# Optimization experiments

Measured on AMD Instinct MI355X. Metric: run time of the kernel, lower is better.

The kernel has to match this reference:

```python
import jax, jax.numpy as jnp
import numpy as np

B, N, D = 8, 2048, 512
DK, DV = 512, 512


def setup_inputs() -> dict:
    key = jax.random.key(0)
    ks = jax.random.split(key, 7)
    s = 1.0 / np.sqrt(D)
    return {
        "x": jax.random.normal(ks[0], (B, N, D), dtype=jnp.float32),
        "Wq": jax.random.normal(ks[1], (D, DK), dtype=jnp.float32) * s,
        "bq": jnp.zeros((DK,), dtype=jnp.float32),
        "Wk": jax.random.normal(ks[2], (D, DK), dtype=jnp.float32) * s,
        "bk": jnp.zeros((DK,), dtype=jnp.float32),
        "Wv": jax.random.normal(ks[3], (D, DV), dtype=jnp.float32) * s,
        "bv": jnp.zeros((DV,), dtype=jnp.float32),
    }


def reference(x, Wq, bq, Wk, bk, Wv, bv):
    # norm = 1/sqrt(dim_k); original divides softmax output by norm (post-softmax scale)
    inv_norm = jnp.sqrt(jnp.asarray(DK, dtype=x.dtype))  # 1/norm = sqrt(dim_k)
    Q = x @ Wq + bq  # [B,N,DK]
    K = x @ Wk + bk  # [B,N,DK]
    V = x @ Wv + bv  # [B,N,DV]
    scores = jnp.einsum("bnd,bmd->bnm", Q, K)  # [B,N,N] (NO pre-softmax scaling)
    att = jax.nn.softmax(scores, axis=-1) * inv_norm  # faithful post-softmax scale
    return jnp.einsum("bnm,bmv->bnv", att, V)  # [B,N,DV]
```

## Files before the change

kernel.cpp:

```cpp
#include <hip/hip_runtime.h>
#include <stdint.h>
#include <stddef.h>


typedef _Float16 f16_t;
typedef _Float16 f16x8 __attribute__((ext_vector_type(8)));
typedef float    f32x4 __attribute__((ext_vector_type(4)));

__device__ __forceinline__ f32x4 mfma_h(f16x8 a, f16x8 b, f32x4 c) {
  return __builtin_amdgcn_mfma_f32_16x16x32_f16(a, b, c, 0, 0, 0);
}

__device__ __forceinline__ void gl_lds16(const void* g, void* lds) {
  __builtin_amdgcn_global_load_lds(
      (const __attribute__((address_space(1))) unsigned int*)g,
      (__attribute__((address_space(3))) unsigned int*)lds, 16, 0, 0);
}

__device__ __forceinline__ void stage_tile(f16_t* lds, const f16_t* g,
                                           size_t gstride, int wave, int lane) {
  const int l8 = lane >> 3;
  const int lslot = (lane & 7) ^ l8;
  #pragma unroll
  for (int c = 0; c < 4; ++c) {
    const int chunk = wave * 4 + c;
    const int row = chunk * 8 + l8;
    gl_lds16(g + (size_t)row * gstride + lslot * 8, lds + chunk * 512);
  }
}

__device__ __forceinline__ f16x8 lds_frag(const f16_t* buf, int R, int slot) {
  return *(const f16x8*)&buf[R * 64 + (((slot ^ (R & 7)) & 7) << 3)];
}

__device__ __forceinline__ unsigned int fenc(float f) {
  unsigned int u = __float_as_uint(f);
  return (u & 0x80000000u) ? ~u : (u | 0x80000000u);
}
__device__ __forceinline__ float fdec(unsigned int e) {
  unsigned int u = (e & 0x80000000u) ? (e & 0x7fffffffu) : ~e;
  return __uint_as_float(u);
}

__device__ __forceinline__ int xcd_swz(int id, int nwg) {
  return (id & 7) * (nwg >> 3) + (id >> 3);
}

__global__ __launch_bounds__(256) void k_conv_x(const float* __restrict__ x,
                                                f16_t* __restrict__ x16) {
  const int i = (blockIdx.x * 256 + threadIdx.x) * 8;
  const float4 a = *(const float4*)&x[i];
  const float4 b = *(const float4*)&x[i + 4];
  float v[8] = {a.x, a.y, a.z, a.w, b.x, b.y, b.z, b.w};
  f16x8 h;
  #pragma unroll
  for (int j = 0; j < 8; ++j) h[j] = (f16_t)v[j];
  *(f16x8*)&x16[i] = h;
}

__global__ __launch_bounds__(256) void k_conv_w(const float* __restrict__ Wq,
                                                const float* __restrict__ Wk,
                                                const float* __restrict__ Wv,
                                                f16_t* __restrict__ Wt) {
  __shared__ float t[64][65];
  const int p = blockIdx.z;
  const float* __restrict__ W = (p == 0) ? Wq : (p == 1) ? Wk : Wv;
  const int n0 = blockIdx.x * 64, k0 = blockIdx.y * 64;
  const int tx = threadIdx.x & 63, ty = threadIdx.x >> 6;
  #pragma unroll
  for (int j = 0; j < 16; ++j)
    t[ty * 16 + j][tx] = W[(size_t)(k0 + ty * 16 + j) * 512 + n0 + tx];
  __syncthreads();
  #pragma unroll
  for (int j = 0; j < 16; ++j) {
    const int nl = ty * 16 + j;
    Wt[(size_t)p * 262144 + (size_t)(n0 + nl) * 512 + k0 + tx] =
        (f16_t)t[tx][nl];
  }
}

__global__ __launch_bounds__(256, 2) void k_proj(
    const f16_t* __restrict__ x16, const f16_t* __restrict__ Wt,
    const float* __restrict__ bq, const float* __restrict__ bk,
    const float* __restrict__ bv,
    f16_t* __restrict__ Q, f16_t* __restrict__ K, f16_t* __restrict__ Vt)
{
  __shared__ __align__(16) unsigned char smem[34816];
  f16_t* A = (f16_t*)smem;
  f16_t* B = (f16_t*)(smem + 16384);

  const int wg = xcd_swz(blockIdx.x, 1536);
  const int mt = wg / 12, jt = wg % 12;
  const int which = jt >> 2;
  const int jb = (jt & 3) * 128;

  const int tid = threadIdx.x, lane = tid & 63, wave = tid >> 6;
  const int wr = wave >> 1, wc = wave & 1, l15 = lane & 15, lg = lane >> 4;
  const int rowbase = mt * 128;

  const f16_t* Wbase = Wt + (size_t)which * 262144 + (size_t)jb * 512;

  f32x4 acc[4][4] = {};

  for (int kb = 0; kb < 512; kb += 64) {
    __syncthreads();
    stage_tile(A, x16 + (size_t)rowbase * 512 + kb, 512, wave, lane);
    stage_tile(B, Wbase + kb, 512, wave, lane);
    __syncthreads();
    #pragma unroll
    for (int h = 0; h < 2; ++h) {
      const int slot0 = h * 4 + lg;
      f16x8 af[4], bf[4];
      #pragma unroll
      for (int g = 0; g < 4; ++g) {
        af[g] = lds_frag(A, wr * 64 + g * 16 + l15, slot0);
        bf[g] = lds_frag(B, wc * 64 + g * 16 + l15, slot0);
      }
      #pragma unroll
      for (int i = 0; i < 4; ++i)
        #pragma unroll
        for (int j = 0; j < 4; ++j)
          acc[i][j] = mfma_h(af[i], bf[j], acc[i][j]);
    }
  }

  if (which != 2) {
    f16_t* __restrict__ O = (which == 0) ? Q : K;
    const float* __restrict__ bb = (which == 0) ? bq : bk;
    #pragma unroll
    for (int j = 0; j < 4; ++j) {
      const int jl = jb + wc * 64 + j * 16 + l15;
      const float bias = bb[jl];
      #pragma unroll
      for (int i = 0; i < 4; ++i)
        #pragma unroll
        for (int r = 0; r < 4; ++r) {
          const int row = rowbase + wr * 64 + i * 16 + lg * 4 + r;
          O[(size_t)row * 512 + jl] = (f16_t)(acc[i][j][r] + bias);
        }
    }
  } else {
    __syncthreads();
    f16_t* vtl = (f16_t*)smem;
    #pragma unroll
    for (int j = 0; j < 4; ++j) {
      const int jj = wc * 64 + j * 16 + l15;
      const float bias = bv[jb + jj];
      #pragma unroll
      for (int i = 0; i < 4; ++i)
        #pragma unroll
        for (int r = 0; r < 4; ++r) {
          const int ii = wr * 64 + i * 16 + lg * 4 + r;
          vtl[jj * 136 + ii] = (f16_t)(acc[i][j][r] + bias);
        }
    }
    __syncthreads();
    const int dv = tid >> 1, hf = tid & 1;
    const int bat = rowbase >> 11, n0 = rowbase & 2047;
    f16_t* __restrict__ dst =
        &Vt[((size_t)bat * 512 + jb + dv) * 2048 + n0 + hf * 64];
    const f16_t* src = &vtl[dv * 136 + hf * 64];
    #pragma unroll
    for (int s = 0; s < 8; ++s)
      *(f16x8*)&dst[s * 8] = *(const f16x8*)&src[s * 8];
  }
}

__global__ __launch_bounds__(256, 2) void k_qk(const f16_t* __restrict__ Q,
                                               const f16_t* __restrict__ K,
                                               float* __restrict__ S,
                                               unsigned int* __restrict__ mEnc)
{
  __shared__ __align__(16) f16_t A[128 * 64];
  __shared__ __align__(16) f16_t Bt[128 * 64];

  const int wg = xcd_swz(blockIdx.x, 2048);
  const int bat = wg >> 8, mt = (wg >> 4) & 15, nt = wg & 15;
  const int tid = threadIdx.x, lane = tid & 63, wave = tid >> 6;
  const int wr = wave >> 1, wc = wave & 1, l15 = lane & 15, lg = lane >> 4;

  f32x4 acc[4][4] = {};
  const f16_t* Abase = Q + ((size_t)bat * 2048 + mt * 128) * 512;
  const f16_t* Bbase = K + ((size_t)bat * 2048 + nt * 128) * 512;

  for (int kb = 0; kb < 512; kb += 64) {
    __syncthreads();
    stage_tile(A, Abase + kb, 512, wave, lane);
    stage_tile(Bt, Bbase + kb, 512, wave, lane);
    __syncthreads();
    #pragma unroll
    for (int h = 0; h < 2; ++h) {
      const int slot0 = h * 4 + lg;
      f16x8 af[4], bf[4];
      #pragma unroll
      for (int g = 0; g < 4; ++g) {
        af[g] = lds_frag(A, wr * 64 + g * 16 + l15, slot0);
        bf[g] = lds_frag(Bt, wc * 64 + g * 16 + l15, slot0);
      }
      #pragma unroll
      for (int i = 0; i < 4; ++i)
        #pragma unroll
        for (int j = 0; j < 4; ++j)
          acc[i][j] = mfma_h(af[i], bf[j], acc[i][j]);
    }
  }

  #pragma unroll
  for (int i = 0; i < 4; ++i)
    #pragma unroll
    for (int r = 0; r < 4; ++r) {
      const int ii = mt * 128 + wr * 64 + i * 16 + lg * 4 + r;
      float mv = fmaxf(fmaxf(acc[i][0][r], acc[i][1][r]),
                       fmaxf(acc[i][2][r], acc[i][3][r]));
      mv = fmaxf(mv, __shfl_xor(mv, 1));
      mv = fmaxf(mv, __shfl_xor(mv, 2));
      mv = fmaxf(mv, __shfl_xor(mv, 4));
      mv = fmaxf(mv, __shfl_xor(mv, 8));
      if (l15 == 0)
        atomicMax(&mEnc[(size_t)bat * 2048 + ii], fenc(mv));
      #pragma unroll
      for (int j = 0; j < 4; ++j) {
        const int jj = nt * 128 + wc * 64 + j * 16 + l15;
        S[((size_t)bat * 2048 + ii) * 2048 + jj] = acc[i][j][r];
      }
    }
}

__global__ __launch_bounds__(256, 2) void k_pv2(const float* __restrict__ S,
                                                const f16_t* __restrict__ Vt,
                                                const unsigned int* __restrict__ mEnc,
                                                float* __restrict__ out)
{
  __shared__ __align__(16) f16_t P[64 * 64];
  __shared__ __align__(16) f16_t Vl[256 * 64];
  __shared__ float lred[64][4];

  const int id = blockIdx.x;
  const int bat = id & 7, qt = (id >> 3) & 31, dvh = id >> 8;
  const int tid = threadIdx.x, lane = tid & 63, wave = tid >> 6;
  const int l15 = lane & 15, lg = lane >> 4;

  const int qs = tid >> 2;
  const int cq = tid & 3;
  const float mrow = fdec(mEnc[bat * 2048 + qt * 64 + qs]);
  const float* __restrict__ srow =
      S + ((size_t)bat * 2048 + qt * 64 + qs) * 2048;
  const f16_t* Vbase = Vt + ((size_t)bat * 512 + dvh * 256) * 2048;

  f32x4 acc[4][4] = {};
  float l_part = 0.f;

  for (int kb = 0; kb < 2048; kb += 64) {
    __syncthreads();
    stage_tile(Vl, Vbase + kb, 2048, wave, lane);
    stage_tile(Vl + 128 * 64, Vbase + (size_t)128 * 2048 + kb, 2048, wave, lane);
    #pragma unroll
    for (int s2 = 0; s2 < 2; ++s2) {
      const int kv0 = cq * 16 + s2 * 8;
      const float4 a = *(const float4*)&srow[kb + kv0];
      const float4 b = *(const float4*)&srow[kb + kv0 + 4];
      float e[8] = {a.x, a.y, a.z, a.w, b.x, b.y, b.z, b.w};
      f16x8 p;
      #pragma unroll
      for (int j = 0; j < 8; ++j) {
        const float ev = __expf(e[j] - mrow);
        l_part += ev;
        p[j] = (f16_t)ev;
      }
      const int slot = cq * 2 + s2;
      *(f16x8*)&P[qs * 64 + ((slot ^ (qs & 7)) << 3)] = p;
    }
    __syncthreads();
    #pragma unroll
    for (int ks = 0; ks < 2; ++ks) {
      const int slot0 = ks * 4 + lg;
      f16x8 af[4], bf[4];
      #pragma unroll
      for (int g = 0; g < 4; ++g) {
        af[g] = lds_frag(P, g * 16 + l15, slot0);
        bf[g] = lds_frag(Vl, wave * 64 + g * 16 + l15, slot0);
      }
      #pragma unroll
      for (int i = 0; i < 4; ++i)
        #pragma unroll
        for (int j = 0; j < 4; ++j)
          acc[i][j] = mfma_h(af[i], bf[j], acc[i][j]);
    }
  }

  __syncthreads();
  lred[qs][cq] = l_part;
  __syncthreads();

  #pragma unroll
  for (int i = 0; i < 4; ++i)
    #pragma unroll
    for (int r = 0; r < 4; ++r) {
      const int ql = i * 16 + lg * 4 + r;
      const float l = lred[ql][0] + lred[ql][1] + lred[ql][2] + lred[ql][3];
      const float sc = 22.62741699796952f / l;
      const size_t orow = ((size_t)bat * 2048 + qt * 64 + ql) * 512;
      #pragma unroll
      for (int j = 0; j < 4; ++j) {
        const int dv = dvh * 256 + wave * 64 + j * 16 + l15;
        out[orow + dv] = acc[i][j][r] * sc;
      }
    }
}

extern "C" void kernel_launch(void* const* d_in, const int* in_sizes, int n_in,
                              void* d_out, int out_size, void* d_ws, size_t ws_size,
                              hipStream_t stream) {
  const float* x  = (const float*)d_in[0];
  const float* Wq = (const float*)d_in[1];
  const float* bq = (const float*)d_in[2];
  const float* Wk = (const float*)d_in[3];
  const float* bk = (const float*)d_in[4];
  const float* Wv = (const float*)d_in[5];
  const float* bv = (const float*)d_in[6];
  float* out = (float*)d_out;

  char* ws = (char*)d_ws;
  f16_t* x16 = (f16_t*)(ws + 0);
  f16_t* Q   = (f16_t*)(ws + 16777216);
  f16_t* K   = (f16_t*)(ws + 33554432);
  f16_t* Vt  = (f16_t*)(ws + 50331648);
  float* S   = (float*)(ws + 67108864);
  f16_t* Wt  = (f16_t*)(ws + 201326592);
  unsigned int* mEnc = (unsigned int*)(ws + 202899456);

  hipMemsetAsync(mEnc, 0, 65536, stream);
  k_conv_x<<<4096, 256, 0, stream>>>(x, x16);
  k_conv_w<<<dim3(8, 8, 3), 256, 0, stream>>>(Wq, Wk, Wv, Wt);
  k_proj<<<1536, 256, 0, stream>>>(x16, Wt, bq, bk, bv, Q, K, Vt);
  k_qk<<<2048, 256, 0, stream>>>(Q, K, S, mEnc);
  k_pv2<<<512, 256, 0, stream>>>(S, Vt, mEnc, out);
}
```

Before: 160.1 us.

## Compute tile-local softmax in QK kernel and store fp16 probabilities with per-tile stats

New measurement: 159.0 us. About the same (-0.7%).

```diff
diff --git a/kernel.cpp b/kernel.cpp
--- a/kernel.cpp
+++ b/kernel.cpp
@@ -29,17 +29,20 @@
   }
 }
 
+__device__ __forceinline__ void stage_tile64(f16_t* lds, const f16_t* g,
+                                             size_t gstride, int wave, int lane) {
+  const int l8 = lane >> 3;
+  const int lslot = (lane & 7) ^ l8;
+  #pragma unroll
+  for (int c = 0; c < 2; ++c) {
+    const int chunk = wave * 2 + c;
+    const int row = chunk * 8 + l8;
+    gl_lds16(g + (size_t)row * gstride + lslot * 8, lds + chunk * 512);
+  }
+}
+
 __device__ __forceinline__ f16x8 lds_frag(const f16_t* buf, int R, int slot) {
   return *(const f16x8*)&buf[R * 64 + (((slot ^ (R & 7)) & 7) << 3)];
-}
-
-__device__ __forceinline__ unsigned int fenc(float f) {
-  unsigned int u = __float_as_uint(f);
-  return (u & 0x80000000u) ? ~u : (u | 0x80000000u);
-}
-__device__ __forceinline__ float fdec(unsigned int e) {
-  unsigned int u = (e & 0x80000000u) ? (e & 0x7fffffffu) : ~e;
-  return __uint_as_float(u);
 }
 
 __device__ __forceinline__ int xcd_swz(int id, int nwg) {
@@ -166,13 +169,17 @@
   }
 }
 
-__global__ __launch_bounds__(256, 2) void k_qk(const f16_t* __restrict__ Q,
-                                               const f16_t* __restrict__ K,
-                                               float* __restrict__ S,
-                                               unsigned int* __restrict__ mEnc)
+__global__ __launch_bounds__(256, 2) void k_qk2(const f16_t* __restrict__ Q,
+                                                const f16_t* __restrict__ K,
+                                                f16_t* __restrict__ P,
+                                                float* __restrict__ mG,
+                                                float* __restrict__ lG)
 {
-  __shared__ __align__(16) f16_t A[128 * 64];
-  __shared__ __align__(16) f16_t Bt[128 * 64];
+  __shared__ __align__(16) unsigned char smem[34816];
+  f16_t* A  = (f16_t*)smem;
+  f16_t* Bt = (f16_t*)(smem + 16384);
+  __shared__ float redm[128][2];
+  __shared__ float redl[128][2];
 
   const int wg = xcd_swz(blockIdx.x, 2048);
   const int bat = wg >> 8, mt = (wg >> 4) & 15, nt = wg & 15;
@@ -205,100 +212,159 @@
     }
   }
 
+  const float LOG2E = 1.4426950408889634f;
   #pragma unroll
   for (int i = 0; i < 4; ++i)
     #pragma unroll
     for (int r = 0; r < 4; ++r) {
-      const int ii = mt * 128 + wr * 64 + i * 16 + lg * 4 + r;
       float mv = fmaxf(fmaxf(acc[i][0][r], acc[i][1][r]),
                        fmaxf(acc[i][2][r], acc[i][3][r]));
       mv = fmaxf(mv, __shfl_xor(mv, 1));
       mv = fmaxf(mv, __shfl_xor(mv, 2));
       mv = fmaxf(mv, __shfl_xor(mv, 4));
       mv = fmaxf(mv, __shfl_xor(mv, 8));
-      if (l15 == 0)
-        atomicMax(&mEnc[(size_t)bat * 2048 + ii], fenc(mv));
+      if (l15 == 0) redm[wr * 64 + i * 16 + lg * 4 + r][wc] = mv;
+    }
+  __syncthreads();
+
+  f16_t* Pl = (f16_t*)smem;
+  #pragma unroll
+  for (int i = 0; i < 4; ++i)
+    #pragma unroll
+    for (int r = 0; r < 4; ++r) {
+      const int rl = wr * 64 + i * 16 + lg * 4 + r;
+      const float m = fmaxf(redm[rl][0], redm[rl][1]);
+      float sum = 0.f;
       #pragma unroll
       for (int j = 0; j < 4; ++j) {
-        const int jj = nt * 128 + wc * 64 + j * 16 + l15;
-        S[((size_t)bat * 2048 + ii) * 2048 + jj] = acc[i][j][r];
-      }
-    }
-}
-
-__global__ __launch_bounds__(256, 2) void k_pv2(const float* __restrict__ S,
+        const float e =
+            __builtin_amdgcn_exp2f((acc[i][j][r] - m) * LOG2E);
+        const f16_t h = (f16_t)e;
+        Pl[rl * 136 + wc * 64 + j * 16 + l15] = h;
+        sum += (float)h;
+      }
+      sum += __shfl_xor(sum, 1);
+      sum += __shfl_xor(sum, 2);
+      sum += __shfl_xor(sum, 4);
+      sum += __shfl_xor(sum, 8);
+      if (l15 == 0) redl[rl][wc] = sum;
+    }
+  __syncthreads();
+
+  if (wc == 0 && l15 == 0) {
+    #pragma unroll
+    for (int i = 0; i < 4; ++i)
+      #pragma unroll
+      for (int r = 0; r < 4; ++r) {
+        const int rl = wr * 64 + i * 16 + lg * 4 + r;
+        const size_t idx =
+            ((size_t)(bat * 16 + nt)) * 2048 + mt * 128 + rl;
+        mG[idx] = fmaxf(redm[rl][0], redm[rl][1]);
+        lG[idx] = redl[rl][0] + redl[rl][1];
+      }
+  }
+
+  {
+    const int row = tid >> 1, half = tid & 1;
+    f16_t* __restrict__ dst =
+        P + ((size_t)bat * 2048 + mt * 128 + row) * 2048 + nt * 128 + half * 64;
+    const f16_t* src = &Pl[row * 136 + half * 64];
+    #pragma unroll
+    for (int s = 0; s < 8; ++s)
+      *(f16x8*)&dst[s * 8] = *(const f16x8*)&src[s * 8];
+  }
+}
+
+__global__ __launch_bounds__(256, 2) void k_pv5(const f16_t* __restrict__ P,
                                                 const f16_t* __restrict__ Vt,
-                                                const unsigned int* __restrict__ mEnc,
+                                                const float* __restrict__ mG,
+                                                const float* __restrict__ lG,
                                                 float* __restrict__ out)
 {
-  __shared__ __align__(16) f16_t P[64 * 64];
+  __shared__ __align__(16) f16_t Pl[64 * 64];
   __shared__ __align__(16) f16_t Vl[256 * 64];
-  __shared__ float lred[64][4];
+  __shared__ f16_t facL[64][16];
+  __shared__ float scrow[64];
+  __shared__ float redp[64][4];
 
   const int id = blockIdx.x;
   const int bat = id & 7, qt = (id >> 3) & 31, dvh = id >> 8;
   const int tid = threadIdx.x, lane = tid & 63, wave = tid >> 6;
   const int l15 = lane & 15, lg = lane >> 4;
-
-  const int qs = tid >> 2;
-  const int cq = tid & 3;
-  const float mrow = fdec(mEnc[bat * 2048 + qt * 64 + qs]);
-  const float* __restrict__ srow =
-      S + ((size_t)bat * 2048 + qt * 64 + qs) * 2048;
+  const float LOG2E = 1.4426950408889634f;
+
+  {
+    const int prow = tid >> 2, part = tid & 3;
+    float mt4[4], lt4[4];
+    #pragma unroll
+    for (int s = 0; s < 4; ++s) {
+      const size_t idx =
+          ((size_t)(bat * 16 + part * 4 + s)) * 2048 + qt * 64 + prow;
+      mt4[s] = mG[idx];
+      lt4[s] = lG[idx];
+    }
+    float mm = fmaxf(fmaxf(mt4[0], mt4[1]), fmaxf(mt4[2], mt4[3]));
+    redp[prow][part] = mm;
+    __syncthreads();
+    const float M = fmaxf(fmaxf(redp[prow][0], redp[prow][1]),
+                          fmaxf(redp[prow][2], redp[prow][3]));
+    __syncthreads();
+    float ls = 0.f;
+    #pragma unroll
+    for (int s = 0; s < 4; ++s) {
+      const float f = __builtin_amdgcn_exp2f((mt4[s] - M) * LOG2E);
+      facL[prow][part * 4 + s] = (f16_t)f;
+      ls += lt4[s] * f;
+    }
+    redp[prow][part] = ls;
+    __syncthreads();
+    if (part == 0)
+      scrow[prow] = 22.62741699796952f /
+                    (redp[prow][0] + redp[prow][1] + redp[prow][2] + redp[prow][3]);
+  }
+
+  const f16_t* Pbase = P + ((size_t)bat * 2048 + qt * 64) * 2048;
   const f16_t* Vbase = Vt + ((size_t)bat * 512 + dvh * 256) * 2048;
 
   f32x4 acc[4][4] = {};
-  float l_part = 0.f;
-
-  for (int kb = 0; kb < 2048; kb += 64) {
-    __syncthreads();
-    stage_tile(Vl, Vbase + kb, 2048, wave, lane);
-    stage_tile(Vl + 128 * 64, Vbase + (size_t)128 * 2048 + kb, 2048, wave, lane);
-    #pragma unroll
-    for (int s2 = 0; s2 < 2; ++s2) {
-      const int kv0 = cq * 16 + s2 * 8;
-      const float4 a = *(const float4*)&srow[kb + kv0];
-      const float4 b = *(const float4*)&srow[kb + kv0 + 4];
-      float e[8] = {a.x, a.y, a.z, a.w, b.x, b.y, b.z, b.w};
-      f16x8 p;
-      #pragma unroll
-      for (int j = 0; j < 8; ++j) {
-        const float ev = __expf(e[j] - mrow);
-        l_part += ev;
-        p[j] = (f16_t)ev;
-      }
-      const int slot = cq * 2 + s2;
-      *(f16x8*)&P[qs * 64 + ((slot ^ (qs & 7)) << 3)] = p;
-    }
-    __syncthreads();
-    #pragma unroll
-    for (int ks = 0; ks < 2; ++ks) {
-      const int slot0 = ks * 4 + lg;
-      f16x8 af[4], bf[4];
-      #pragma unroll
-      for (int g = 0; g < 4; ++g) {
-        af[g] = lds_frag(P, g * 16 + l15, slot0);
-        bf[g] = lds_frag(Vl, wave * 64 + g * 16 + l15, slot0);
-      }
-      #pragma unroll
-      for (int i = 0; i < 4; ++i)
-        #pragma unroll
-        for (int j = 0; j < 4; ++j)
-          acc[i][j] = mfma_h(af[i], bf[j], acc[i][j]);
-    }
-  }
-
-  __syncthreads();
-  lred[qs][cq] = l_part;
-  __syncthreads();
+
+  for (int tt = 0; tt < 16; ++tt) {
+    f16_t fv[4];
+    #pragma unroll
+    for (int g = 0; g < 4; ++g) fv[g] = facL[g * 16 + l15][tt];
+
+    #pragma unroll
+    for (int h2 = 0; h2 < 2; ++h2) {
+      const int kb = tt * 128 + h2 * 64;
+      __syncthreads();
+      stage_tile(Vl, Vbase + kb, 2048, wave, lane);
+      stage_tile(Vl + 128 * 64, Vbase + (size_t)128 * 2048 + kb, 2048, wave, lane);
+      stage_tile64(Pl, Pbase + kb, 2048, wave, lane);
+      __syncthreads();
+      #pragma unroll
+      for (int ks = 0; ks < 2; ++ks) {
+        const int slot0 = ks * 4 + lg;
+        f16x8 af[4], bf[4];
+        #pragma unroll
+        for (int g = 0; g < 4; ++g) {
+          af[g] = lds_frag(Pl, g * 16 + l15, slot0) * fv[g];
+          bf[g] = lds_frag(Vl, wave * 64 + g * 16 + l15, slot0);
+        }
+        #pragma unroll
+        for (int i = 0; i < 4; ++i)
+          #pragma unroll
+          for (int j = 0; j < 4; ++j)
+            acc[i][j] = mfma_h(af[i], bf[j], acc[i][j]);
+      }
+    }
+  }
 
   #pragma unroll
   for (int i = 0; i < 4; ++i)
     #pragma unroll
     for (int r = 0; r < 4; ++r) {
       const int ql = i * 16 + lg * 4 + r;
-      const float l = lred[ql][0] + lred[ql][1] + lred[ql][2] + lred[ql][3];
-      const float sc = 22.62741699796952f / l;
+      const float sc = scrow[ql];
       const size_t orow = ((size_t)bat * 2048 + qt * 64 + ql) * 512;
       #pragma unroll
       for (int j = 0; j < 4; ++j) {
@@ -325,14 +391,14 @@
   f16_t* Q   = (f16_t*)(ws + 16777216);
   f16_t* K   = (f16_t*)(ws + 33554432);
   f16_t* Vt  = (f16_t*)(ws + 50331648);
-  float* S   = (float*)(ws + 67108864);
+  f16_t* P   = (f16_t*)(ws + 67108864);
+  float* mG  = (float*)(ws + 134217728);
+  float* lG  = (float*)(ws + 136314880);
   f16_t* Wt  = (f16_t*)(ws + 201326592);
-  unsigned int* mEnc = (unsigned int*)(ws + 202899456);
-
-  hipMemsetAsync(mEnc, 0, 65536, stream);
+
   k_conv_x<<<4096, 256, 0, stream>>>(x, x16);
   k_conv_w<<<dim3(8, 8, 3), 256, 0, stream>>>(Wq, Wk, Wv, Wt);
   k_proj<<<1536, 256, 0, stream>>>(x16, Wt, bq, bk, bv, Q, K, Vt);
-  k_qk<<<2048, 256, 0, stream>>>(Q, K, S, mEnc);
-  k_pv2<<<512, 256, 0, stream>>>(S, Vt, mEnc, out);
-}
+  k_qk2<<<2048, 256, 0, stream>>>(Q, K, P, mG, lG);
+  k_pv5<<<512, 256, 0, stream>>>(P, Vt, mG, lG, out);
+}
```
